# Optimization experiments

Measured on AMD Instinct MI355X. Metric: run time of the kernel, lower is better.

## Reference

```python
import jax, jax.numpy as jnp
import numpy as np
import math

D_MODEL = 1024
EXPAND = 2
D_INNER = EXPAND * D_MODEL  # 2048
D_STATE = 16
D_CONV = 4
DT_RANK = math.ceil(D_MODEL / 16)  # 64
BATCH = 1
SEQLEN = 2048


def _silu(x):
    return x * jax.nn.sigmoid(x)


def _selective_scan(u, delta, A, B, C, D, z, delta_bias):
    """u, delta, z: (b,d,l); A: (d,n); B, C: (b,n,l); D, delta_bias: (d)."""
    delta = jax.nn.softplus(delta + delta_bias[None, :, None])        # (b,d,l)
    dA = jnp.exp(jnp.einsum('bdl,dn->lbdn', delta, A))                # (l,b,d,n)
    dBu = jnp.einsum('bdl,bnl->lbdn', delta * u, B)                   # (l,b,d,n)
    Ct = jnp.transpose(C, (2, 0, 1))                                  # (l,b,n)

    def step(h, inp):
        dA_t, dBu_t, C_t = inp
        h = dA_t * h + dBu_t                                          # (b,d,n)
        y = jnp.einsum('bdn,bn->bd', h, C_t)
        return h, y

    h0 = jnp.zeros((u.shape[0], u.shape[1], A.shape[1]), dtype=u.dtype)
    _, ys = jax.lax.scan(step, h0, (dA, dBu, Ct))                     # ys: (l,b,d)
    y = jnp.transpose(ys, (1, 2, 0))                                  # (b,d,l)
    y = y + D[:, None] * u
    return y * _silu(z)


def _causal_conv1d(x, conv_w, conv_b):
    """x: (b,d,l); conv_w: (d,w); conv_b: (d). Depthwise causal conv."""
    x_pad = jnp.pad(x, ((0, 0), (0, 0), (D_CONV - 1, 0)))
    kernel = conv_w[:, None, :]  # (d, 1, w)
    y = jax.lax.conv_general_dilated(
        x_pad, kernel, window_strides=(1,), padding='VALID',
        dimension_numbers=('NCH', 'OIH', 'NCH'),
        feature_group_count=D_INNER)
    return y + conv_b[None, :, None]


def setup_inputs() -> dict:
    key = jax.random.key(0)
    ks = jax.random.split(key, 12)
    hidden_states = jax.random.normal(ks[0], (BATCH, SEQLEN, D_MODEL), dtype=jnp.float32)
    in_proj_w = jax.random.normal(ks[1], (2 * D_INNER, D_MODEL), dtype=jnp.float32) * (D_MODEL ** -0.5)
    conv_w = jax.random.normal(ks[2], (D_INNER, D_CONV), dtype=jnp.float32) * (D_CONV ** -0.5)
    conv_b = jnp.zeros((D_INNER,), dtype=jnp.float32)
    dt_std = DT_RANK ** -0.5

    def dt_bias(k):
        dt = jnp.exp(jax.random.uniform(k, (D_INNER,)) * (math.log(0.1) - math.log(0.001)) + math.log(0.001))
        dt = jnp.clip(dt, 1e-4, None)
        return dt + jnp.log(-jnp.expm1(-dt))  # inverse softplus

    A_log = jnp.log(jnp.broadcast_to(jnp.arange(1, D_STATE + 1, dtype=jnp.float32), (D_INNER, D_STATE)))
    x1_proj_w = jax.random.normal(ks[3], (DT_RANK + 2 * D_STATE, D_INNER), dtype=jnp.float32) * (D_INNER ** -0.5)
    dt1_proj_w = jax.random.uniform(ks[4], (D_INNER, DT_RANK), minval=-dt_std, maxval=dt_std)
    dt1_proj_b = dt_bias(ks[5])
    x2_proj_w = jax.random.normal(ks[6], (DT_RANK + 2 * D_STATE, D_INNER), dtype=jnp.float32) * (D_INNER ** -0.5)
    dt2_proj_w = jax.random.uniform(ks[7], (D_INNER, DT_RANK), minval=-dt_std, maxval=dt_std)
    dt2_proj_b = dt_bias(ks[8])
    out_proj_w = jax.random.normal(ks[9], (D_MODEL, D_INNER), dtype=jnp.float32) * (D_INNER ** -0.5)
    return {
        'hidden_states': hidden_states,
        'in_proj_w': in_proj_w, 'conv_w': conv_w, 'conv_b': conv_b,
        'x1_proj_w': x1_proj_w, 'dt1_proj_w': dt1_proj_w, 'dt1_proj_b': dt1_proj_b,
        'A1_log': A_log, 'D1': jnp.ones((D_INNER,), dtype=jnp.float32),
        'x2_proj_w': x2_proj_w, 'dt2_proj_w': dt2_proj_w, 'dt2_proj_b': dt2_proj_b,
        'A2_log': A_log, 'D2': jnp.ones((D_INNER,), dtype=jnp.float32),
        'out_proj_w': out_proj_w,
    }


def reference(hidden_states, in_proj_w, conv_w, conv_b,
              x1_proj_w, dt1_proj_w, dt1_proj_b, A1_log, D1,
              x2_proj_w, dt2_proj_w, dt2_proj_b, A2_log, D2,
              out_proj_w):
    # in_proj: (b,l,d) @ W^T -> (b, 2*d_inner, l)
    xz = jnp.einsum('bld,ed->bel', hidden_states, in_proj_w)
    x, z = jnp.split(xz, 2, axis=1)                                   # (b,d_inner,l) each
    A1 = -jnp.exp(A1_log.astype(jnp.float32))
    A2 = -jnp.exp(A2_log.astype(jnp.float32))
    x = _silu(_causal_conv1d(x, conv_w, conv_b))                      # (b,d_inner,l)

    def branch_params(xp_w, dtp_w):
        dbl = jnp.einsum('bdl,kd->bkl', x, xp_w)                      # (b, r+2n, l)
        dt, Bm, Cm = jnp.split(dbl, [DT_RANK, DT_RANK + D_STATE], axis=1)
        dt = jnp.einsum('brl,dr->bdl', dt, dtp_w)
        return dt, Bm, Cm

    dt1, B1, C1 = branch_params(x1_proj_w, dt1_proj_w)
    dt2, B2, C2 = branch_params(x2_proj_w, dt2_proj_w)
    y1 = _selective_scan(x, dt1, A1, B1, C1, D1.astype(jnp.float32), z, dt1_proj_b.astype(jnp.float32))
    y2 = _selective_scan(x, dt2, A2, B2, C2, D2.astype(jnp.float32), z, dt2_proj_b.astype(jnp.float32))
    y = y1 - y2                                                       # (b,d_inner,l)
    out = jnp.einsum('bdl,od->blo', y, out_proj_w)                    # (b,l,d_model)
    return out
```

## Files before the change

kernel.cpp:

```cpp
#include <hip/hip_runtime.h>
#include <math.h>

#define SEQ 2048
#define DMODEL 1024
#define DIN 2048
#define NST 16
#define DTR 64
#define CH 32
#define NCH (SEQ / CH)
#define LOG2E 1.4426950408889634f

typedef __attribute__((ext_vector_type(8))) _Float16 f16x8;
typedef __attribute__((ext_vector_type(4))) float f32x4;

__device__ __forceinline__ ushort f2h(float f) {
  union { _Float16 h; ushort u; } c; c.h = (_Float16)f; return c.u;
}
__device__ __forceinline__ float h2f(ushort u) {
  union { ushort u; _Float16 h; } c; c.u = u; return (float)c.h;
}
__device__ __forceinline__ float splus(float v) {
  return v > 20.f ? v : log1pf(__expf(v));
}
__device__ __forceinline__ void powers16(float e, float* p) {
  float e2 = e * e, e4 = e2 * e2, e8 = e4 * e4;
  p[0] = e;       p[1] = e2;       p[2] = e2 * e;   p[3] = e4;
  p[4] = e4 * e;  p[5] = e4 * e2;  p[6] = e4 * p[2]; p[7] = e8;
  p[8] = e8 * e;  p[9] = e8 * e2;  p[10] = e8 * p[2]; p[11] = e8 * e4;
  p[12] = e8 * p[4]; p[13] = e8 * p[5]; p[14] = e8 * p[6]; p[15] = e8 * e8;
}

#define GLL(g, l) __builtin_amdgcn_global_load_lds( \
    (const __attribute__((address_space(1))) void*)(g), \
    (__attribute__((address_space(3))) void*)(l), 16, 0, 0)

template<int BM, int BN, int SPLITK, int MODE>
__global__ __launch_bounds__(256, 2) void gemm3p(const ushort* __restrict__ Ahi,
                                                 const ushort* __restrict__ Alo,
                                                 const ushort* __restrict__ Bhi,
                                                 const ushort* __restrict__ Blo,
                                                 float* __restrict__ C,
                                                 int M, int N, int K) {
  constexpr int BK = 32;
  constexpr int WM = BM / 2, WN = BN / 2, TM = WM / 16, TN = WN / 16;
  constexpr int SA = BM / 16, SB = BN / 16;
  constexpr bool dropB = (MODE == 2);
  __shared__ __align__(16) ushort sAh[BM * BK], sAl[BM * BK];
  __shared__ __align__(16) ushort sBh[BN * BK];
  __shared__ __align__(16) ushort sBl[dropB ? 16 : BN * BK];
  const int tid = threadIdx.x, wid = tid >> 6, lane = tid & 63;
  const int m0 = blockIdx.y * BM, n0 = blockIdx.x * BN;
  const int Kc = K / SPLITK, kbeg = blockIdx.z * Kc;
  const int wm0 = (wid >> 1) * WM, wn0 = (wid & 1) * WN;
  const int fr = lane & 15;
  const int lrow = lane >> 2;
  const int lkc = (lane & 3) ^ ((lane >> 3) & 3);
  const int fpo = fr * 32 + (((lane >> 4) ^ ((lane >> 1) & 3)) * 8);

  f32x4 acc[TM][TN], accL[TM][TN];
#pragma unroll
  for (int mi = 0; mi < TM; ++mi)
#pragma unroll
    for (int ni = 0; ni < TN; ++ni)
#pragma unroll
      for (int r = 0; r < 4; ++r) { acc[mi][ni][r] = 0.f; accL[mi][ni][r] = 0.f; }

  for (int k0 = 0; k0 < Kc; k0 += BK) {
    __syncthreads();
    const int kg = kbeg + k0 + lkc * 8;
#pragma unroll
    for (int i = 0; i < SA / 4; ++i) {
      const int seg = wid * (SA / 4) + i;
      const size_t ga = (size_t)(m0 + seg * 16 + lrow) * K + kg;
      GLL(&Ahi[ga], &sAh[seg * 512]);
      GLL(&Alo[ga], &sAl[seg * 512]);
    }
#pragma unroll
    for (int i = 0; i < SB / 4; ++i) {
      const int seg = wid * (SB / 4) + i;
      const size_t ga = (size_t)(n0 + seg * 16 + lrow) * K + kg;
      GLL(&Bhi[ga], &sBh[seg * 512]);
      if constexpr (!dropB) GLL(&Blo[ga], &sBl[seg * 512]);
    }
    __syncthreads();

    f16x8 ah[TM], al[TM], bh[TN], bl[TN];
#pragma unroll
    for (int mi = 0; mi < TM; ++mi) {
      const int r = (wm0 / 16 + mi) * 512 + fpo;
      ah[mi] = *(const f16x8*)&sAh[r];
      al[mi] = *(const f16x8*)&sAl[r];
    }
#pragma unroll
    for (int ni = 0; ni < TN; ++ni) {
      const int r = (wn0 / 16 + ni) * 512 + fpo;
      bh[ni] = *(const f16x8*)&sBh[r];
      if constexpr (!dropB) bl[ni] = *(const f16x8*)&sBl[r];
    }
#pragma unroll
    for (int mi = 0; mi < TM; ++mi)
#pragma unroll
      for (int ni = 0; ni < TN; ++ni) {
        acc[mi][ni] = __builtin_amdgcn_mfma_f32_16x16x32_f16(ah[mi], bh[ni], acc[mi][ni], 0, 0, 0);
        accL[mi][ni] = __builtin_amdgcn_mfma_f32_16x16x32_f16(al[mi], bh[ni], accL[mi][ni], 0, 0, 0);
        if constexpr (!dropB)
          accL[mi][ni] = __builtin_amdgcn_mfma_f32_16x16x32_f16(ah[mi], bl[ni], accL[mi][ni], 0, 0, 0);
      }
  }

  float* __restrict__ Co = C + (size_t)blockIdx.z * M * N;
#pragma unroll
  for (int mi = 0; mi < TM; ++mi)
#pragma unroll
    for (int ni = 0; ni < TN; ++ni)
#pragma unroll
      for (int r = 0; r < 4; ++r)
        Co[(size_t)(m0 + wm0 + mi * 16 + (lane >> 4) * 4 + r) * N + n0 + wn0 + ni * 16 + fr] =
            acc[mi][ni][r] + accL[mi][ni][r] * (1.f / 2048.f);
}

__device__ __forceinline__ void split_store4h(float4 v, ushort* hi, ushort* lo, size_t i) {
  ushort h0 = f2h(v.x), h1 = f2h(v.y), h2 = f2h(v.z), h3 = f2h(v.w);
  *(ushort4*)&hi[i] = make_ushort4(h0, h1, h2, h3);
  *(ushort4*)&lo[i] = make_ushort4(f2h((v.x - h2f(h0)) * 2048.f), f2h((v.y - h2f(h1)) * 2048.f),
                                   f2h((v.z - h2f(h2)) * 2048.f), f2h((v.w - h2f(h3)) * 2048.f));
}

__global__ __launch_bounds__(256) void cvt_fused(const float* __restrict__ inw,
                                                 const float* __restrict__ hid,
                                                 const float* __restrict__ x1w,
                                                 const float* __restrict__ x2w,
                                                 ushort* __restrict__ w_hi, ushort* __restrict__ w_lo,
                                                 ushort* __restrict__ h_hi,
                                                 ushort* __restrict__ wx_hi, ushort* __restrict__ wx_lo) {
  const int q = blockIdx.x * 256 + threadIdx.x;
  if (q >= 1048576 && q < 1572864) {
    const size_t i = (size_t)(q - 1048576) * 4;
    float4 v = *(const float4*)&hid[i];
    *(ushort4*)&h_hi[i] = make_ushort4(f2h(v.x), f2h(v.y), f2h(v.z), f2h(v.w));
    return;
  }
  const float* src; ushort* dhi; ushort* dlo; int base;
  if (q < 1048576)       { src = inw; dhi = w_hi;  dlo = w_lo;  base = q; }
  else if (q < 1622016)  { src = x1w; dhi = wx_hi; dlo = wx_lo; base = q - 1572864; }
  else                   { src = x2w; dhi = wx_hi + 196608; dlo = wx_lo + 196608; base = q - 1622016; }
  const size_t i = (size_t)base * 4;
  split_store4h(*(const float4*)&src[i], dhi, dlo, i);
}

__global__ __launch_bounds__(256) void reduce_out(const float* __restrict__ p,
                                                  float* __restrict__ o, int n) {
  const int i = (blockIdx.x * 256 + threadIdx.x) * 4;
  if (i >= n) return;
  float4 a = *(const float4*)&p[i];
  float4 b = *(const float4*)&p[(size_t)n + i];
  float4 c = *(const float4*)&p[(size_t)2 * n + i];
  float4 d = *(const float4*)&p[(size_t)3 * n + i];
  *(float4*)&o[i] = make_float4(a.x + b.x + c.x + d.x, a.y + b.y + c.y + d.y,
                                a.z + b.z + c.z + d.z, a.w + b.w + c.w + d.w);
}

__global__ __launch_bounds__(256) void conv_tr_kernel(const float* __restrict__ xz,
                                                      const float* __restrict__ cw,
                                                      const float* __restrict__ cb,
                                                      ushort* __restrict__ xcT_hi,
                                                      ushort* __restrict__ xcT_lo,
                                                      float* __restrict__ zsT) {
  const int l0 = blockIdx.x * 64, d0 = blockIdx.y * 64;
  const int tid = threadIdx.x;
  __shared__ float xin[64][68];
  __shared__ float To[64][65];
  __shared__ float cwS[64][4];
  __shared__ float cbS[64];

  for (int i = tid; i < 1024; i += 256) {
    const int d = i >> 4, q = i & 15;
    float4 v = *(const float4*)&xz[(size_t)(d0 + d) * SEQ + l0 + q * 4];
    xin[d][3 + q * 4 + 0] = v.x; xin[d][3 + q * 4 + 1] = v.y;
    xin[d][3 + q * 4 + 2] = v.z; xin[d][3 + q * 4 + 3] = v.w;
  }
  if (tid < 192) {
    const int j = tid >> 6, d = tid & 63;
    const int l = l0 - 3 + j;
    xin[d][j] = (l >= 0) ? xz[(size_t)(d0 + d) * SEQ + l] : 0.f;
  }
  if (tid < 64) {
    cbS[tid] = cb[d0 + tid];
    float4 w = *(const float4*)&cw[(d0 + tid) * 4];
    cwS[tid][0] = w.x; cwS[tid][1] = w.y; cwS[tid][2] = w.z; cwS[tid][3] = w.w;
  }
  __syncthreads();

  for (int i = tid; i < 4096; i += 256) {
    const int d = i >> 6, l = i & 63;
    float a = cbS[d] + cwS[d][0] * xin[d][l] + cwS[d][1] * xin[d][l + 1] +
              cwS[d][2] * xin[d][l + 2] + cwS[d][3] * xin[d][l + 3];
    To[d][l] = a / (1.f + __expf(-a));
  }
  __syncthreads();

  for (int i = tid; i < 4096; i += 256) {
    const int l = i >> 6, dd = i & 63;
    float v = To[dd][l];
    ushort h = f2h(v);
    xcT_hi[(size_t)(l0 + l) * DIN + d0 + dd] = h;
    xcT_lo[(size_t)(l0 + l) * DIN + d0 + dd] = f2h((v - h2f(h)) * 2048.f);
  }
  __syncthreads();

  for (int i = tid; i < 1024; i += 256) {
    const int d = i >> 4, q = i & 15;
    float4 v = *(const float4*)&xz[(size_t)(DIN + d0 + d) * SEQ + l0 + q * 4];
    To[d][q * 4 + 0] = v.x / (1.f + __expf(-v.x));
    To[d][q * 4 + 1] = v.y / (1.f + __expf(-v.y));
    To[d][q * 4 + 2] = v.z / (1.f + __expf(-v.z));
    To[d][q * 4 + 3] = v.w / (1.f + __expf(-v.w));
  }
  __syncthreads();
  for (int i = tid; i < 4096; i += 256) {
    const int l = i >> 6, dd = i & 63;
    zsT[(size_t)(l0 + l) * DIN + d0 + dd] = To[dd][l];
  }
}

__global__ __launch_bounds__(256) void reduce_dblS_kernel(const float* __restrict__ p,
                                                          float* __restrict__ o,
                                                          float* __restrict__ BT1,
                                                          float* __restrict__ CT1,
                                                          float* __restrict__ BT2,
                                                          float* __restrict__ CT2) {
  const int NE = 192 * SEQ;
  const int idx = blockIdx.x * 256 + threadIdx.x;
  float s = 0.f;
#pragma unroll
  for (int cc = 0; cc < 8; ++cc) s += p[(size_t)cc * NE + idx];
  o[idx] = s;
  const int k = idx >> 11, l = idx & (SEQ - 1);
  if (k >= 64 && k < 80)        BT1[l * NST + (k - 64)] = s;
  else if (k >= 80 && k < 96)   CT1[l * NST + (k - 80)] = s;
  else if (k >= 160 && k < 176) BT2[l * NST + (k - 160)] = s;
  else if (k >= 176)            CT2[l * NST + (k - 176)] = s;
}

__global__ __launch_bounds__(256) void dt_gemm_kernel(const float* __restrict__ dbl1,
                                                      const float* __restrict__ dbl2,
                                                      const float* __restrict__ w1,
                                                      const float* __restrict__ w2,
                                                      const float* __restrict__ b1,
                                                      const float* __restrict__ b2,
                                                      float* __restrict__ o1,
                                                      float* __restrict__ o2) {
  const int br = blockIdx.z;
  const float* __restrict__ dbl = br ? dbl2 : dbl1;
  const float* __restrict__ W = br ? w2 : w1;
  const float* __restrict__ dtb = br ? b2 : b1;
  float* __restrict__ outp = br ? o2 : o1;
  const int l0 = blockIdx.x * 64, d0 = blockIdx.y * 64;
  __shared__ __align__(16) float Wt[64][68];
  __shared__ __align__(16) float Bs[64][68];
  const int tid = threadIdx.x;
  for (int i = tid; i < 4096; i += 256) {
    int a = i >> 6, b = i & 63;
    Wt[b][a] = W[(size_t)(d0 + a) * DTR + b];
    Bs[a][b] = dbl[(size_t)a * SEQ + l0 + b];
  }
  __syncthreads();
  const int tl_ = tid >> 4, td_ = tid & 15;
  float acc[4][4];
#pragma unroll
  for (int i = 0; i < 4; ++i)
#pragma unroll
    for (int j = 0; j < 4; ++j) acc[i][j] = 0.f;
  for (int r = 0; r < 64; ++r) {
    float4 av = *(const float4*)&Bs[r][tl_ * 4];
    float4 bv = *(const float4*)&Wt[r][td_ * 4];
    float am[4] = {av.x, av.y, av.z, av.w};
    float bn[4] = {bv.x, bv.y, bv.z, bv.w};
#pragma unroll
    for (int i = 0; i < 4; ++i)
#pragma unroll
      for (int j = 0; j < 4; ++j) acc[i][j] = fmaf(am[i], bn[j], acc[i][j]);
  }
  const float4 bias4 = *(const float4*)&dtb[d0 + td_ * 4];
#pragma unroll
  for (int i = 0; i < 4; ++i) {
    float4 w = make_float4(splus(acc[i][0] + bias4.x), splus(acc[i][1] + bias4.y),
                           splus(acc[i][2] + bias4.z), splus(acc[i][3] + bias4.w));
    *(float4*)&outp[(size_t)(l0 + tl_ * 4 + i) * DIN + d0 + td_ * 4] = w;
  }
}

__global__ __launch_bounds__(256) void scan_phase_a(const ushort* __restrict__ uhi,
                                                    const ushort* __restrict__ ulo,
                                                    const float* __restrict__ sp1T,
                                                    const float* __restrict__ sp2T,
                                                    const float* __restrict__ BT1,
                                                    const float* __restrict__ BT2,
                                                    const float* __restrict__ Al1,
                                                    const float* __restrict__ Al2,
                                                    float* __restrict__ hend,
                                                    float* __restrict__ Pend) {
  const int c = blockIdx.y, t0 = c * CH;
  const int d = blockIdx.x * 256 + threadIdx.x;
  const size_t gbase = (size_t)t0 * DIN + d;

  __shared__ __align__(16) float Bs[2][CH][NST];
  {
    const int j = threadIdx.x;
    if (j < 128) ((float4*)&Bs[0][0][0])[j] = ((const float4*)&BT1[(size_t)t0 * NST])[j];
    else ((float4*)&Bs[1][0][0])[j - 128] = ((const float4*)&BT2[(size_t)t0 * NST])[j - 128];
  }
  __syncthreads();

  bool fast = true;
#pragma unroll
  for (int n = 0; n < NST; ++n) {
    float k1 = __expf(Al1[(size_t)d * NST + n]);
    float k2 = __expf(Al2[(size_t)d * NST + n]);
    fast = fast && (fabsf(k1 - (float)(n + 1)) < 1e-3f) && (fabsf(k2 - (float)(n + 1)) < 1e-3f);
  }
  float h1[NST], h2[NST];
#pragma unroll
  for (int n = 0; n < NST; ++n) { h1[n] = 0.f; h2[n] = 0.f; }
  float S1 = 0.f, S2 = 0.f;

  if (fast) {
    for (int tt = 0; tt < CH / 4; ++tt) {
      float s1[4], s2[4], ua[4];
#pragma unroll
      for (int j = 0; j < 4; ++j) {
        const size_t idx = gbase + (size_t)(tt * 4 + j) * DIN;
        s1[j] = sp1T[idx]; s2[j] = sp2T[idx];
        ua[j] = h2f(uhi[idx]) + h2f(ulo[idx]) * (1.f / 2048.f);
      }
#pragma unroll
      for (int j = 0; j < 4; ++j) {
        const int t = tt * 4 + j;
        S1 += s1[j]; S2 += s2[j];
        const float spu1 = s1[j] * ua[j], spu2 = s2[j] * ua[j];
        float p[NST];
        powers16(__expf(-s1[j]), p);
#pragma unroll
        for (int n = 0; n < NST; ++n) h1[n] = fmaf(p[n], h1[n], spu1 * Bs[0][t][n]);
        powers16(__expf(-s2[j]), p);
#pragma unroll
        for (int n = 0; n < NST; ++n) h2[n] = fmaf(p[n], h2[n], spu2 * Bs[1][t][n]);
      }
    }
  } else {
    float A1e[NST], A2e[NST];
#pragma unroll
    for (int n = 0; n < NST; ++n) {
      A1e[n] = -__expf(Al1[(size_t)d * NST + n]) * LOG2E;
      A2e[n] = -__expf(Al2[(size_t)d * NST + n]) * LOG2E;
    }
    for (int tt = 0; tt < CH / 4; ++tt) {
      float s1[4], s2[4], ua[4];
#pragma unroll
      for (int j = 0; j < 4; ++j) {
        const size_t idx = gbase + (size_t)(tt * 4 + j) * DIN;
        s1[j] = sp1T[idx]; s2[j] = sp2T[idx];
        ua[j] = h2f(uhi[idx]) + h2f(ulo[idx]) * (1.f / 2048.f);
      }
#pragma unroll
      for (int j = 0; j < 4; ++j) {
        const int t = tt * 4 + j;
        S1 += s1[j]; S2 += s2[j];
        const float spu1 = s1[j] * ua[j], spu2 = s2[j] * ua[j];
#pragma unroll
        for (int n = 0; n < NST; ++n) {
          h1[n] = fmaf(exp2f(A1e[n] * s1[j]), h1[n], spu1 * Bs[0][t][n]);
          h2[n] = fmaf(exp2f(A2e[n] * s2[j]), h2[n], spu2 * Bs[1][t][n]);
        }
      }
    }
  }

  float P1[NST], P2[NST];
  if (fast) {
    powers16(__expf(-S1), P1);
    powers16(__expf(-S2), P2);
  } else {
#pragma unroll
    for (int n = 0; n < NST; ++n) {
      P1[n] = exp2f(-__expf(Al1[(size_t)d * NST + n]) * LOG2E * S1);
      P2[n] = exp2f(-__expf(Al2[(size_t)d * NST + n]) * LOG2E * S2);
    }
  }
  const size_t b1 = ((size_t)c * DIN + d) * NST;
  const size_t b2 = ((size_t)(NCH + c) * DIN + d) * NST;
#pragma unroll
  for (int n = 0; n < NST; n += 4) {
    *(float4*)&hend[b1 + n] = make_float4(h1[n], h1[n + 1], h1[n + 2], h1[n + 3]);
    *(float4*)&Pend[b1 + n] = make_float4(P1[n], P1[n + 1], P1[n + 2], P1[n + 3]);
    *(float4*)&hend[b2 + n] = make_float4(h2[n], h2[n + 1], h2[n + 2], h2[n + 3]);
    *(float4*)&Pend[b2 + n] = make_float4(P2[n], P2[n + 1], P2[n + 2], P2[n + 3]);
  }
}

__global__ __launch_bounds__(256) void carry_cvt(const float* __restrict__ hend,
                                                 float* __restrict__ PendHin,
                                                 const float* __restrict__ outw,
                                                 ushort* __restrict__ ow_hi) {
  const int b = blockIdx.x;
  if (b < 256) {
    const int flat = b * 256 + threadIdx.x;
    const int br = flat >> 15;
    const int dn = flat & 32767;
    float h = 0.f;
    for (int c = 0; c < NCH; ++c) {
      size_t idx = ((size_t)(br * NCH + c) << 15) + dn;
      float Pv = PendHin[idx];
      float he = hend[idx];
      PendHin[idx] = h;
      h = fmaf(Pv, h, he);
    }
  } else {
    const size_t i = ((size_t)(b - 256) * 256 + threadIdx.x) * 4;
    float4 v = *(const float4*)&outw[i];
    *(ushort4*)&ow_hi[i] = make_ushort4(f2h(v.x), f2h(v.y), f2h(v.z), f2h(v.w));
  }
}

__global__ __launch_bounds__(256) void scan_phase_c(const ushort* __restrict__ uhi,
                                                    const ushort* __restrict__ ulo,
                                                    const float* __restrict__ sp1T,
                                                    const float* __restrict__ sp2T,
                                                    const float* __restrict__ BT1,
                                                    const float* __restrict__ CT1,
                                                    const float* __restrict__ BT2,
                                                    const float* __restrict__ CT2,
                                                    const float* __restrict__ Al1,
                                                    const float* __restrict__ Al2,
                                                    const float* __restrict__ D1,
                                                    const float* __restrict__ D2,
                                                    const float* __restrict__ hin,
                                                    const float* __restrict__ zsT,
                                                    ushort* __restrict__ yd_hi,
                                                    ushort* __restrict__ yd_lo) {
  const int c = blockIdx.y, t0 = c * CH;
  const int d = blockIdx.x * 256 + threadIdx.x;
  const size_t gbase = (size_t)t0 * DIN + d;

  __shared__ __align__(16) float Bs[2][CH][NST];
  __shared__ __align__(16) float Cs[2][CH][NST];
  {
    const int j = threadIdx.x;
    if (j < 128) {
      ((float4*)&Bs[0][0][0])[j] = ((const float4*)&BT1[(size_t)t0 * NST])[j];
      ((float4*)&Cs[0][0][0])[j] = ((const float4*)&CT1[(size_t)t0 * NST])[j];
    } else {
      ((float4*)&Bs[1][0][0])[j - 128] = ((const float4*)&BT2[(size_t)t0 * NST])[j - 128];
      ((float4*)&Cs[1][0][0])[j - 128] = ((const float4*)&CT2[(size_t)t0 * NST])[j - 128];
    }
  }
  __syncthreads();

  bool fast = true;
#pragma unroll
  for (int n = 0; n < NST; ++n) {
    float k1 = __expf(Al1[(size_t)d * NST + n]);
    float k2 = __expf(Al2[(size_t)d * NST + n]);
    fast = fast && (fabsf(k1 - (float)(n + 1)) < 1e-3f) && (fabsf(k2 - (float)(n + 1)) < 1e-3f);
  }
  const float Ddd = D1[d] - D2[d];
  float h1[NST], h2[NST];
  const size_t hb1 = ((size_t)c * DIN + d) * NST;
  const size_t hb2 = ((size_t)(NCH + c) * DIN + d) * NST;
#pragma unroll
  for (int n = 0; n < NST; n += 4) {
    float4 v1 = *(const float4*)&hin[hb1 + n];
    h1[n] = v1.x; h1[n + 1] = v1.y; h1[n + 2] = v1.z; h1[n + 3] = v1.w;
    float4 v2 = *(const float4*)&hin[hb2 + n];
    h2[n] = v2.x; h2[n + 1] = v2.y; h2[n + 2] = v2.z; h2[n + 3] = v2.w;
  }

  if (fast) {
    for (int tt = 0; tt < CH / 4; ++tt) {
      float s1[4], s2[4], ua[4];
#pragma unroll
      for (int j = 0; j < 4; ++j) {
        const size_t idx = gbase + (size_t)(tt * 4 + j) * DIN;
        s1[j] = sp1T[idx]; s2[j] = sp2T[idx];
        ua[j] = h2f(uhi[idx]) + h2f(ulo[idx]) * (1.f / 2048.f);
      }
#pragma unroll
      for (int j = 0; j < 4; ++j) {
        const int t = tt * 4 + j;
        const size_t idx = gbase + (size_t)t * DIN;
        const float spu1 = s1[j] * ua[j], spu2 = s2[j] * ua[j];
        float p[NST];
        float y1 = 0.f, y2 = 0.f;
        powers16(__expf(-s1[j]), p);
#pragma unroll
        for (int n = 0; n < NST; ++n) {
          h1[n] = fmaf(p[n], h1[n], spu1 * Bs[0][t][n]);
          y1 = fmaf(h1[n], Cs[0][t][n], y1);
        }
        powers16(__expf(-s2[j]), p);
#pragma unroll
        for (int n = 0; n < NST; ++n) {
          h2[n] = fmaf(p[n], h2[n], spu2 * Bs[1][t][n]);
          y2 = fmaf(h2[n], Cs[1][t][n], y2);
        }
        const float yd = (y1 - y2 + Ddd * ua[j]) * zsT[idx];
        const ushort hh = f2h(yd);
        yd_hi[idx] = hh;
        yd_lo[idx] = f2h((yd - h2f(hh)) * 2048.f);
      }
    }
  } else {
    float A1e[NST], A2e[NST];
#pragma unroll
    for (int n = 0; n < NST; ++n) {
      A1e[n] = -__expf(Al1[(size_t)d * NST + n]) * LOG2E;
      A2e[n] = -__expf(Al2[(size_t)d * NST + n]) * LOG2E;
    }
    for (int tt = 0; tt < CH / 4; ++tt) {
      float s1[4], s2[4], ua[4];
#pragma unroll
      for (int j = 0; j < 4; ++j) {
        const size_t idx = gbase + (size_t)(tt * 4 + j) * DIN;
        s1[j] = sp1T[idx]; s2[j] = sp2T[idx];
        ua[j] = h2f(uhi[idx]) + h2f(ulo[idx]) * (1.f / 2048.f);
      }
#pragma unroll
      for (int j = 0; j < 4; ++j) {
        const int t = tt * 4 + j;
        const size_t idx = gbase + (size_t)t * DIN;
        const float spu1 = s1[j] * ua[j], spu2 = s2[j] * ua[j];
        float y1 = 0.f, y2 = 0.f;
#pragma unroll
        for (int n = 0; n < NST; ++n) {
          h1[n] = fmaf(exp2f(A1e[n] * s1[j]), h1[n], spu1 * Bs[0][t][n]);
          y1 = fmaf(h1[n], Cs[0][t][n], y1);
          h2[n] = fmaf(exp2f(A2e[n] * s2[j]), h2[n], spu2 * Bs[1][t][n]);
          y2 = fmaf(h2[n], Cs[1][t][n], y2);
        }
        const float yd = (y1 - y2 + Ddd * ua[j]) * zsT[idx];
        const ushort hh = f2h(yd);
        yd_hi[idx] = hh;
        yd_lo[idx] = f2h((yd - h2f(hh)) * 2048.f);
      }
    }
  }
}

extern "C" void kernel_launch(void* const* d_in, const int* in_sizes, int n_in,
                              void* d_out, int out_size, void* d_ws, size_t ws_size,
                              hipStream_t stream) {
  const float* hidden = (const float*)d_in[0];
  const float* in_proj_w = (const float*)d_in[1];
  const float* conv_w = (const float*)d_in[2];
  const float* conv_b = (const float*)d_in[3];
  const float* x1w = (const float*)d_in[4];
  const float* dtw1 = (const float*)d_in[5];
  const float* dtb1 = (const float*)d_in[6];
  const float* Al1 = (const float*)d_in[7];
  const float* D1 = (const float*)d_in[8];
  const float* x2w = (const float*)d_in[9];
  const float* dtw2 = (const float*)d_in[10];
  const float* dtb2 = (const float*)d_in[11];
  const float* Al2 = (const float*)d_in[12];
  const float* D2 = (const float*)d_in[13];
  const float* outw = (const float*)d_in[14];
  float* out = (float*)d_out;

  float* ws = (float*)d_ws;
  float* xz = ws;
  float* xcTbuf = xz + (size_t)4096 * SEQ;
  float* dblS = xcTbuf + (size_t)SEQ * DIN;
  float* sp1T = dblS + (size_t)192 * SEQ;
  float* sp2T = sp1T + (size_t)SEQ * DIN;
  float* siluzT = sp2T + (size_t)SEQ * DIN;
  float* hendB = siluzT + (size_t)SEQ * DIN;
  float* PendB = hendB + (size_t)2 * NCH * DIN * NST;
  float* BT1 = PendB + (size_t)2 * NCH * DIN * NST;
  float* CT1 = BT1 + (size_t)SEQ * NST;
  float* BT2 = CT1 + (size_t)SEQ * NST;
  float* CT2 = BT2 + (size_t)SEQ * NST;
  float* wxp = CT2 + (size_t)SEQ * NST;

  float* dbl1 = dblS;
  float* dbl2 = dblS + (size_t)96 * SEQ;

  ushort* xcT_hi = (ushort*)xcTbuf;
  ushort* xcT_lo = (ushort*)(xcTbuf + 2097152);
  ushort* w_hi = (ushort*)siluzT;
  ushort* w_lo = (ushort*)(siluzT + 2097152);
  ushort* h_hi = (ushort*)hendB;
  ushort* wx_hi = (ushort*)wxp;
  ushort* wx_lo = (ushort*)(wxp + 196608);
  float* xp_part = sp1T;
  ushort* yd_hi = (ushort*)xcTbuf;
  ushort* yd_lo = (ushort*)(xcTbuf + 2097152);
  ushort* ow_hi = (ushort*)xz;
  float* opart = sp1T;

  dim3 blk(256);

  cvt_fused<<<dim3(6528), blk, 0, stream>>>(in_proj_w, hidden, x1w, x2w,
                                            w_hi, w_lo, h_hi, wx_hi, wx_lo);

  gemm3p<128, 128, 1, 2><<<dim3(SEQ / 128, 4096 / 128, 1), blk, 0, stream>>>(
      w_hi, w_lo, h_hi, h_hi, xz, 4096, SEQ, DMODEL);

  conv_tr_kernel<<<dim3(SEQ / 64, DIN / 64), blk, 0, stream>>>(
      xz, conv_w, conv_b, xcT_hi, xcT_lo, siluzT);

  gemm3p<64, 128, 8, 0><<<dim3(SEQ / 128, 192 / 64, 8), blk, 0, stream>>>(
      wx_hi, wx_lo, xcT_hi, xcT_lo, xp_part, 192, SEQ, DIN);

  reduce_dblS_kernel<<<dim3(192 * SEQ / 256), blk, 0, stream>>>(
      xp_part, dblS, BT1, CT1, BT2, CT2);

  dt_gemm_kernel<<<dim3(SEQ / 64, DIN / 64, 2), blk, 0, stream>>>(
      dbl1, dbl2, dtw1, dtw2, dtb1, dtb2, sp1T, sp2T);

  scan_phase_a<<<dim3(DIN / 256, NCH), blk, 0, stream>>>(
      xcT_hi, xcT_lo, sp1T, sp2T, BT1, BT2, Al1, Al2, hendB, PendB);
  carry_cvt<<<dim3(2304), blk, 0, stream>>>(hendB, PendB, outw, ow_hi);
  scan_phase_c<<<dim3(DIN / 256, NCH), blk, 0, stream>>>(
      xcT_hi, xcT_lo, sp1T, sp2T, BT1, CT1, BT2, CT2, Al1, Al2, D1, D2,
      PendB, siluzT, yd_hi, yd_lo);

  gemm3p<128, 128, 4, 2><<<dim3(DMODEL / 128, SEQ / 128, 4), blk, 0, stream>>>(
      yd_hi, yd_lo, ow_hi, ow_hi, opart, SEQ, DMODEL, DIN);
  reduce_out<<<dim3(SEQ * DMODEL / 1024), blk, 0, stream>>>(opart, out, SEQ * DMODEL);
}
```

Before: 332.5 us.

## Move dt projection to split-fp16 MFMA GEMM and transpose x_proj output layout

Replaces the scalar FP32 dt projection GEMM with an MFMA kernel that uses hi/lo fp16 splitting (three MFMAs per tile) and fuses bias plus softplus into its epilogue. The x_proj GEMM operands are swapped so it produces an (l, k) layout. The reduce kernel then writes dt as transposed hi/lo fp16 directly, and the dt weights are converted in the existing conversion kernel. This removes FP32 FMA work and transposed shared-memory loads. The cost is extra conversion passes and a small loss of precision from the split-fp16 approximation.

```diff
diff --git a/kernel.cpp b/kernel.cpp
--- a/kernel.cpp
+++ b/kernel.cpp
@@ -119,6 +119,91 @@
             acc[mi][ni][r] + accL[mi][ni][r] * (1.f / 2048.f);
 }
 
+__global__ __launch_bounds__(256, 2) void dt_mfma(const ushort* __restrict__ dtT_hi,
+                                                  const ushort* __restrict__ dtT_lo,
+                                                  const ushort* __restrict__ dw_hi,
+                                                  const ushort* __restrict__ dw_lo,
+                                                  const float* __restrict__ b1,
+                                                  const float* __restrict__ b2,
+                                                  float* __restrict__ o1,
+                                                  float* __restrict__ o2) {
+  const int br = blockIdx.z;
+  const ushort* __restrict__ Ah = dtT_hi + (size_t)br * 131072;
+  const ushort* __restrict__ Al_ = dtT_lo + (size_t)br * 131072;
+  const ushort* __restrict__ Bh = dw_hi + (size_t)br * 131072;
+  const ushort* __restrict__ Bl = dw_lo + (size_t)br * 131072;
+  const float* __restrict__ bias = br ? b2 : b1;
+  float* __restrict__ o = br ? o2 : o1;
+  __shared__ __align__(16) ushort sAh[128 * 32], sAl[128 * 32];
+  __shared__ __align__(16) ushort sBh[128 * 32], sBl[128 * 32];
+  const int tid = threadIdx.x, wid = tid >> 6, lane = tid & 63;
+  const int m0 = blockIdx.y * 128, n0 = blockIdx.x * 128;
+  const int wm0 = (wid >> 1) * 64, wn0 = (wid & 1) * 64;
+  const int fr = lane & 15;
+  const int lrow = lane >> 2;
+  const int lkc = (lane & 3) ^ ((lane >> 3) & 3);
+  const int fpo = fr * 32 + (((lane >> 4) ^ ((lane >> 1) & 3)) * 8);
+
+  f32x4 acc[4][4], accL[4][4];
+#pragma unroll
+  for (int mi = 0; mi < 4; ++mi)
+#pragma unroll
+    for (int ni = 0; ni < 4; ++ni)
+#pragma unroll
+      for (int r = 0; r < 4; ++r) { acc[mi][ni][r] = 0.f; accL[mi][ni][r] = 0.f; }
+
+  for (int k0 = 0; k0 < 64; k0 += 32) {
+    __syncthreads();
+    const int kg = k0 + lkc * 8;
+#pragma unroll
+    for (int i = 0; i < 2; ++i) {
+      const int seg = wid * 2 + i;
+      const size_t ga = (size_t)(m0 + seg * 16 + lrow) * 64 + kg;
+      GLL(&Ah[ga], &sAh[seg * 512]);
+      GLL(&Al_[ga], &sAl[seg * 512]);
+      const size_t gb = (size_t)(n0 + seg * 16 + lrow) * 64 + kg;
+      GLL(&Bh[gb], &sBh[seg * 512]);
+      GLL(&Bl[gb], &sBl[seg * 512]);
+    }
+    __syncthreads();
+
+    f16x8 ah[4], al[4], bh[4], bl[4];
+#pragma unroll
+    for (int mi = 0; mi < 4; ++mi) {
+      const int r = (wm0 / 16 + mi) * 512 + fpo;
+      ah[mi] = *(const f16x8*)&sAh[r];
+      al[mi] = *(const f16x8*)&sAl[r];
+    }
+#pragma unroll
+    for (int ni = 0; ni < 4; ++ni) {
+      const int r = (wn0 / 16 + ni) * 512 + fpo;
+      bh[ni] = *(const f16x8*)&sBh[r];
+      bl[ni] = *(const f16x8*)&sBl[r];
+    }
+#pragma unroll
+    for (int mi = 0; mi < 4; ++mi)
+#pragma unroll
+      for (int ni = 0; ni < 4; ++ni) {
+        acc[mi][ni] = __builtin_amdgcn_mfma_f32_16x16x32_f16(ah[mi], bh[ni], acc[mi][ni], 0, 0, 0);
+        accL[mi][ni] = __builtin_amdgcn_mfma_f32_16x16x32_f16(al[mi], bh[ni], accL[mi][ni], 0, 0, 0);
+        accL[mi][ni] = __builtin_amdgcn_mfma_f32_16x16x32_f16(ah[mi], bl[ni], accL[mi][ni], 0, 0, 0);
+      }
+  }
+
+#pragma unroll
+  for (int ni = 0; ni < 4; ++ni) {
+    const int n = n0 + wn0 + ni * 16 + fr;
+    const float bv = bias[n];
+#pragma unroll
+    for (int mi = 0; mi < 4; ++mi)
+#pragma unroll
+      for (int r = 0; r < 4; ++r) {
+        const int m = m0 + wm0 + mi * 16 + (lane >> 4) * 4 + r;
+        o[(size_t)m * DIN + n] = splus(acc[mi][ni][r] + accL[mi][ni][r] * (1.f / 2048.f) + bv);
+      }
+  }
+}
+
 __device__ __forceinline__ void split_store4h(float4 v, ushort* hi, ushort* lo, size_t i) {
   ushort h0 = f2h(v.x), h1 = f2h(v.y), h2 = f2h(v.z), h3 = f2h(v.w);
   *(ushort4*)&hi[i] = make_ushort4(h0, h1, h2, h3);
@@ -130,9 +215,12 @@
                                                  const float* __restrict__ hid,
                                                  const float* __restrict__ x1w,
                                                  const float* __restrict__ x2w,
+                                                 const float* __restrict__ dtw1,
+                                                 const float* __restrict__ dtw2,
                                                  ushort* __restrict__ w_hi, ushort* __restrict__ w_lo,
                                                  ushort* __restrict__ h_hi,
-                                                 ushort* __restrict__ wx_hi, ushort* __restrict__ wx_lo) {
+                                                 ushort* __restrict__ wx_hi, ushort* __restrict__ wx_lo,
+                                                 ushort* __restrict__ dw_hi, ushort* __restrict__ dw_lo) {
   const int q = blockIdx.x * 256 + threadIdx.x;
   if (q >= 1048576 && q < 1572864) {
     const size_t i = (size_t)(q - 1048576) * 4;
@@ -143,7 +231,9 @@
   const float* src; ushort* dhi; ushort* dlo; int base;
   if (q < 1048576)       { src = inw; dhi = w_hi;  dlo = w_lo;  base = q; }
   else if (q < 1622016)  { src = x1w; dhi = wx_hi; dlo = wx_lo; base = q - 1572864; }
-  else                   { src = x2w; dhi = wx_hi + 196608; dlo = wx_lo + 196608; base = q - 1622016; }
+  else if (q < 1671168)  { src = x2w; dhi = wx_hi + 196608; dlo = wx_lo + 196608; base = q - 1622016; }
+  else if (q < 1703936)  { src = dtw1; dhi = dw_hi; dlo = dw_lo; base = q - 1671168; }
+  else                   { src = dtw2; dhi = dw_hi + 131072; dlo = dw_lo + 131072; base = q - 1703936; }
   const size_t i = (size_t)base * 4;
   split_store4h(*(const float4*)&src[i], dhi, dlo, i);
 }
@@ -223,71 +313,32 @@
   }
 }
 
-__global__ __launch_bounds__(256) void reduce_dblS_kernel(const float* __restrict__ p,
-                                                          float* __restrict__ o,
+__global__ __launch_bounds__(256) void reduce_dblT_kernel(const float* __restrict__ p,
                                                           float* __restrict__ BT1,
                                                           float* __restrict__ CT1,
                                                           float* __restrict__ BT2,
-                                                          float* __restrict__ CT2) {
-  const int NE = 192 * SEQ;
+                                                          float* __restrict__ CT2,
+                                                          ushort* __restrict__ dtT_hi,
+                                                          ushort* __restrict__ dtT_lo) {
+  const int NE = SEQ * 192;
   const int idx = blockIdx.x * 256 + threadIdx.x;
   float s = 0.f;
 #pragma unroll
   for (int cc = 0; cc < 8; ++cc) s += p[(size_t)cc * NE + idx];
-  o[idx] = s;
-  const int k = idx >> 11, l = idx & (SEQ - 1);
-  if (k >= 64 && k < 80)        BT1[l * NST + (k - 64)] = s;
-  else if (k >= 80 && k < 96)   CT1[l * NST + (k - 80)] = s;
-  else if (k >= 160 && k < 176) BT2[l * NST + (k - 160)] = s;
-  else if (k >= 176)            CT2[l * NST + (k - 176)] = s;
-}
-
-__global__ __launch_bounds__(256) void dt_gemm_kernel(const float* __restrict__ dbl1,
-                                                      const float* __restrict__ dbl2,
-                                                      const float* __restrict__ w1,
-                                                      const float* __restrict__ w2,
-                                                      const float* __restrict__ b1,
-                                                      const float* __restrict__ b2,
-                                                      float* __restrict__ o1,
-                                                      float* __restrict__ o2) {
-  const int br = blockIdx.z;
-  const float* __restrict__ dbl = br ? dbl2 : dbl1;
-  const float* __restrict__ W = br ? w2 : w1;
-  const float* __restrict__ dtb = br ? b2 : b1;
-  float* __restrict__ outp = br ? o2 : o1;
-  const int l0 = blockIdx.x * 64, d0 = blockIdx.y * 64;
-  __shared__ __align__(16) float Wt[64][68];
-  __shared__ __align__(16) float Bs[64][68];
-  const int tid = threadIdx.x;
-  for (int i = tid; i < 4096; i += 256) {
-    int a = i >> 6, b = i & 63;
-    Wt[b][a] = W[(size_t)(d0 + a) * DTR + b];
-    Bs[a][b] = dbl[(size_t)a * SEQ + l0 + b];
-  }
-  __syncthreads();
-  const int tl_ = tid >> 4, td_ = tid & 15;
-  float acc[4][4];
-#pragma unroll
-  for (int i = 0; i < 4; ++i)
-#pragma unroll
-    for (int j = 0; j < 4; ++j) acc[i][j] = 0.f;
-  for (int r = 0; r < 64; ++r) {
-    float4 av = *(const float4*)&Bs[r][tl_ * 4];
-    float4 bv = *(const float4*)&Wt[r][td_ * 4];
-    float am[4] = {av.x, av.y, av.z, av.w};
-    float bn[4] = {bv.x, bv.y, bv.z, bv.w};
-#pragma unroll
-    for (int i = 0; i < 4; ++i)
-#pragma unroll
-      for (int j = 0; j < 4; ++j) acc[i][j] = fmaf(am[i], bn[j], acc[i][j]);
-  }
-  const float4 bias4 = *(const float4*)&dtb[d0 + td_ * 4];
-#pragma unroll
-  for (int i = 0; i < 4; ++i) {
-    float4 w = make_float4(splus(acc[i][0] + bias4.x), splus(acc[i][1] + bias4.y),
-                           splus(acc[i][2] + bias4.z), splus(acc[i][3] + bias4.w));
-    *(float4*)&outp[(size_t)(l0 + tl_ * 4 + i) * DIN + d0 + td_ * 4] = w;
-  }
+  const int l = idx / 192, k = idx - l * 192;
+  if (k < 64) {
+    const size_t off = (size_t)l * 64 + k;
+    const ushort hh = f2h(s);
+    dtT_hi[off] = hh; dtT_lo[off] = f2h((s - h2f(hh)) * 2048.f);
+  } else if (k < 80)  BT1[l * NST + (k - 64)] = s;
+  else if (k < 96)    CT1[l * NST + (k - 80)] = s;
+  else if (k < 160) {
+    const size_t off = 131072 + (size_t)l * 64 + (k - 96);
+    const ushort hh = f2h(s);
+    dtT_hi[off] = hh; dtT_lo[off] = f2h((s - h2f(hh)) * 2048.f);
+  }
+  else if (k < 176)   BT2[l * NST + (k - 160)] = s;
+  else                CT2[l * NST + (k - 176)] = s;
 }
 
 __global__ __launch_bounds__(256) void scan_phase_a(const ushort* __restrict__ uhi,
@@ -569,8 +620,8 @@
   float* ws = (float*)d_ws;
   float* xz = ws;
   float* xcTbuf = xz + (size_t)4096 * SEQ;
-  float* dblS = xcTbuf + (size_t)SEQ * DIN;
-  float* sp1T = dblS + (size_t)192 * SEQ;
+  float* dtTbuf = xcTbuf + (size_t)SEQ * DIN;
+  float* sp1T = dtTbuf + (size_t)192 * SEQ;
   float* sp2T = sp1T + (size_t)SEQ * DIN;
   float* siluzT = sp2T + (size_t)SEQ * DIN;
   float* hendB = siluzT + (size_t)SEQ * DIN;
@@ -581,14 +632,15 @@
   float* CT2 = BT2 + (size_t)SEQ * NST;
   float* wxp = CT2 + (size_t)SEQ * NST;
 
-  float* dbl1 = dblS;
-  float* dbl2 = dblS + (size_t)96 * SEQ;
-
   ushort* xcT_hi = (ushort*)xcTbuf;
   ushort* xcT_lo = (ushort*)(xcTbuf + 2097152);
+  ushort* dtT_hi = (ushort*)dtTbuf;
+  ushort* dtT_lo = dtT_hi + 262144;
   ushort* w_hi = (ushort*)siluzT;
   ushort* w_lo = (ushort*)(siluzT + 2097152);
   ushort* h_hi = (ushort*)hendB;
+  ushort* dw_hi = ((ushort*)hendB) + 2097152;
+  ushort* dw_lo = dw_hi + 262144;
   ushort* wx_hi = (ushort*)wxp;
   ushort* wx_lo = (ushort*)(wxp + 196608);
   float* xp_part = sp1T;
@@ -599,8 +651,8 @@
 
   dim3 blk(256);
 
-  cvt_fused<<<dim3(6528), blk, 0, stream>>>(in_proj_w, hidden, x1w, x2w,
-                                            w_hi, w_lo, h_hi, wx_hi, wx_lo);
+  cvt_fused<<<dim3(6784), blk, 0, stream>>>(in_proj_w, hidden, x1w, x2w, dtw1, dtw2,
+                                            w_hi, w_lo, h_hi, wx_hi, wx_lo, dw_hi, dw_lo);
 
   gemm3p<128, 128, 1, 2><<<dim3(SEQ / 128, 4096 / 128, 1), blk, 0, stream>>>(
       w_hi, w_lo, h_hi, h_hi, xz, 4096, SEQ, DMODEL);
@@ -608,14 +660,14 @@
   conv_tr_kernel<<<dim3(SEQ / 64, DIN / 64), blk, 0, stream>>>(
       xz, conv_w, conv_b, xcT_hi, xcT_lo, siluzT);
 
-  gemm3p<64, 128, 8, 0><<<dim3(SEQ / 128, 192 / 64, 8), blk, 0, stream>>>(
-      wx_hi, wx_lo, xcT_hi, xcT_lo, xp_part, 192, SEQ, DIN);
-
-  reduce_dblS_kernel<<<dim3(192 * SEQ / 256), blk, 0, stream>>>(
-      xp_part, dblS, BT1, CT1, BT2, CT2);
-
-  dt_gemm_kernel<<<dim3(SEQ / 64, DIN / 64, 2), blk, 0, stream>>>(
-      dbl1, dbl2, dtw1, dtw2, dtb1, dtb2, sp1T, sp2T);
+  gemm3p<128, 64, 8, 0><<<dim3(192 / 64, SEQ / 128, 8), blk, 0, stream>>>(
+      xcT_hi, xcT_lo, wx_hi, wx_lo, xp_part, SEQ, 192, DIN);
+
+  reduce_dblT_kernel<<<dim3(192 * SEQ / 256), blk, 0, stream>>>(
+      xp_part, BT1, CT1, BT2, CT2, dtT_hi, dtT_lo);
+
+  dt_mfma<<<dim3(DIN / 128, SEQ / 128, 2), blk, 0, stream>>>(
+      dtT_hi, dtT_lo, dw_hi, dw_lo, dtb1, dtb2, sp1T, sp2T);
 
   scan_phase_a<<<dim3(DIN / 256, NCH), blk, 0, stream>>>(
       xcT_hi, xcT_lo, sp1T, sp2T, BT1, BT2, Al1, Al2, hendB, PendB);
```

Measured after the change: 331.7 us. No clear change (-0.2%).
